# Optimization experiments

Hardware: AMD Instinct MI355X
Metric: run time of the kernel (lower is better)

## Reference

```python
import jax, jax.numpy as jnp
import numpy as np

B, S, H = 8, 32, 2048          # batch, block (query) length, hidden size
NH, NKV, HD = 16, 2, 128       # attention heads, kv heads, head_dim
KV_LEN = 8192                  # block kv-cache length
GROUPS = NH // NKV
SCALE = HD ** -0.5


def rotate_half(x):
    x1, x2 = jnp.split(x, 2, axis=-1)
    return jnp.concatenate((-x2, x1), axis=-1)


def setup_inputs() -> dict:
    key = jax.random.key(0)
    ks = jax.random.split(key, 12)
    inv_freq = 1.0 / (10000.0 ** (jnp.arange(0, HD, 2, dtype=jnp.float32) / HD))
    pos = jnp.arange(S, dtype=jnp.float32)[:, None] * inv_freq[None, :]  # [S, HD/2]
    ang = jnp.concatenate([pos, pos], axis=-1)                           # [S, HD]
    cos = jnp.broadcast_to(jnp.cos(ang)[None], (B, S, HD))
    sin = jnp.broadcast_to(jnp.sin(ang)[None], (B, S, HD))
    s = 0.02
    return {
        'hidden_states': jax.random.normal(ks[0], (B, S, H), jnp.float32),
        'cos': cos,
        'sin': sin,
        'k_cache': jax.random.normal(ks[1], (B, NKV, KV_LEN, HD), jnp.float32),
        'v_cache': jax.random.normal(ks[2], (B, NKV, KV_LEN, HD), jnp.float32),
        'attention_mask': jnp.zeros((B, 1, S, KV_LEN), jnp.float32),
        'replace_position': 4096,
        'q_w': jax.random.normal(ks[3], (H, NH * HD), jnp.float32) * s,
        'q_b': jax.random.normal(ks[4], (NH * HD,), jnp.float32) * s,
        'k_w': jax.random.normal(ks[5], (H, NKV * HD), jnp.float32) * s,
        'k_b': jax.random.normal(ks[6], (NKV * HD,), jnp.float32) * s,
        'v_w': jax.random.normal(ks[7], (H, NKV * HD), jnp.float32) * s,
        'v_b': jax.random.normal(ks[8], (NKV * HD,), jnp.float32) * s,
        'o_w': jax.random.normal(ks[9], (NH * HD, H), jnp.float32) * s,
    }


def reference(hidden_states, cos, sin, k_cache, v_cache, attention_mask,
              replace_position, q_w, q_b, k_w, k_b, v_w, v_b, o_w):
    # fused QKV projections -> [B, heads, S, HD]
    q = (hidden_states @ q_w + q_b).reshape(B, S, NH, HD).transpose(0, 2, 1, 3)
    k = (hidden_states @ k_w + k_b).reshape(B, S, NKV, HD).transpose(0, 2, 1, 3)
    v = (hidden_states @ v_w + v_b).reshape(B, S, NKV, HD).transpose(0, 2, 1, 3)

    # RoPE (cos/sin unsqueezed on the head dim)
    c = cos[:, None]  # [B,1,S,HD]
    s_ = sin[:, None]
    q = q * c + rotate_half(q) * s_
    k = k * c + rotate_half(k) * s_

    # block KV-cache in-place update at replace_position
    k_all = jax.lax.dynamic_update_slice(k_cache, k, (0, 0, replace_position, 0))
    v_all = jax.lax.dynamic_update_slice(v_cache, v, (0, 0, replace_position, 0))

    # GQA: expand kv heads to match attention heads
    k_all = jnp.repeat(k_all, GROUPS, axis=1)  # [B,NH,KV,HD]
    v_all = jnp.repeat(v_all, GROUPS, axis=1)

    # SDPA with additive mask (is_causal=False)
    scores = jnp.einsum('bhqd,bhkd->bhqk', q, k_all) * SCALE + attention_mask
    probs = jax.nn.softmax(scores, axis=-1)
    attn = jnp.einsum('bhqk,bhkd->bhqd', probs, v_all)  # [B,NH,S,HD]

    out = attn.transpose(0, 2, 1, 3).reshape(B, S, NH * HD)
    return out @ o_w
```

## Files before the change

### kernel.cpp

```cpp
#include <hip/hip_runtime.h>
#include <hip/hip_bf16.h>

#define B_    8
#define S_    32
#define H_    2048
#define NH_   16
#define NKV_  2
#define HD_   128
#define KV_   8192
#define G_    8
#define M_    256
#define NQKV  2560
#define NSP   16
#define KT_   64
#define NT_   8
#define SCALE_ 0.08838834764831845f
#define CFIX_  8.0f
#define LOG2E_ 1.4426950408889634f
#define SCALE2_ (SCALE_*LOG2E_)

typedef __bf16 bf16x8 __attribute__((ext_vector_type(8)));
typedef float  f32x4  __attribute__((ext_vector_type(4)));
typedef float  f32x16 __attribute__((ext_vector_type(16)));

__device__ __forceinline__ unsigned short f2b(float f){
  unsigned u = __float_as_uint(f);
  u = u + 0x7FFFu + ((u>>16)&1u);
  return (unsigned short)(u>>16);
}
__device__ __forceinline__ float b2f(unsigned short h){
  return __uint_as_float(((unsigned)h)<<16);
}
__device__ __forceinline__ unsigned cvtpk(float lo, float hi){
  unsigned r;
  asm("v_cvt_pk_bf16_f32 %0, %1, %2" : "=v"(r) : "v"(lo), "v"(hi));
  return r;
}
__device__ __forceinline__ float fexp2(float x){
#if __has_builtin(__builtin_amdgcn_exp2f)
  return __builtin_amdgcn_exp2f(x);
#else
  return __expf(x * 0.6931471805599453f);
#endif
}
__device__ __forceinline__ bf16x8 ld_frag(const unsigned short* p){
  union { uint4 u; bf16x8 b; } cv;
  cv.u = *(const uint4*)p;
  return cv.b;
}
__device__ __forceinline__ f32x4 mf(bf16x8 a, bf16x8 b, f32x4 c){
  return __builtin_amdgcn_mfma_f32_16x16x32_bf16(a, b, c, 0, 0, 0);
}
__device__ __forceinline__ f32x16 mf32(bf16x8 a, bf16x8 b, f32x16 c){
  return __builtin_amdgcn_mfma_f32_32x32x16_bf16(a, b, c, 0, 0, 0);
}
__device__ __forceinline__ int swiK(int row, int col){
  return row*128 + (col ^ ((((row)&15) ^ ((row>>1)&8)) << 3));
}
__device__ __forceinline__ int swiV(int row, int col){
  return row*64 + (col ^ (((row)&7) << 3));
}

__global__ __launch_bounds__(256) void k_gemm_qkv(
    const float* __restrict__ A,
    const float* __restrict__ qw, const float* __restrict__ kw, const float* __restrict__ vw,
    const float* __restrict__ qbv, const float* __restrict__ kbv, const float* __restrict__ vbv,
    float* __restrict__ rawp)
{
  __shared__ unsigned short As[64][56];
  __shared__ unsigned short Bs[64][56];
  const int n0 = blockIdx.x*64, m0 = blockIdx.y*64, kz = blockIdx.z;
  const float* W; const float* bias; int ldw, wc0;
  if(n0 < 2048)      { W=qw; bias=qbv; ldw=2048; wc0=n0; }
  else if(n0 < 2304) { W=kw; bias=kbv; ldw=256;  wc0=n0-2048; }
  else               { W=vw; bias=vbv; ldw=256;  wc0=n0-2304; }
  const int t = threadIdx.x, lane = t&63, wid = t>>6;
  const int wr = wid>>1, wc = wid&1, l15 = lane&15, lq = lane>>4;
  const int ar = t>>2,  ac = (t&3)*8;
  const int bk = t>>5,  bn = (t&31)*2;
  f32x4 acc[2][2] = {};
  for(int k0 = kz*512; k0 < kz*512 + 512; k0 += 32){
    __syncthreads();
    { const float4 a0 = *(const float4*)(A + (m0+ar)*2048 + k0 + ac);
      const float4 a1 = *(const float4*)(A + (m0+ar)*2048 + k0 + ac + 4);
      uint4 w4; w4.x=cvtpk(a0.x,a0.y); w4.y=cvtpk(a0.z,a0.w);
                w4.z=cvtpk(a1.x,a1.y); w4.w=cvtpk(a1.z,a1.w);
      *(uint4*)(&As[ar][ac]) = w4; }
    #pragma unroll
    for(int p=0;p<4;p++){
      const int kk = bk + p*8;
      const float2 wv = *(const float2*)(W + (long)(k0+kk)*ldw + wc0 + bn);
      Bs[bn  ][kk] = f2b(wv.x);
      Bs[bn+1][kk] = f2b(wv.y);
    }
    __syncthreads();
    const bf16x8 a0 = ld_frag(&As[wr*32      + l15][lq*8]);
    const bf16x8 a1 = ld_frag(&As[wr*32 + 16 + l15][lq*8]);
    const bf16x8 b0 = ld_frag(&Bs[wc*32      + l15][lq*8]);
    const bf16x8 b1 = ld_frag(&Bs[wc*32 + 16 + l15][lq*8]);
    acc[0][0] = mf(a0,b0,acc[0][0]);
    acc[0][1] = mf(a0,b1,acc[0][1]);
    acc[1][0] = mf(a1,b0,acc[1][0]);
    acc[1][1] = mf(a1,b1,acc[1][1]);
  }
  float* out = rawp + (long)kz*M_*NQKV;
  #pragma unroll
  for(int mi=0;mi<2;mi++)
    #pragma unroll
    for(int nj=0;nj<2;nj++){
      const int col = n0 + wc*32 + nj*16 + l15;
      const float bv = kz ? 0.f : bias[wc0 + wc*32 + nj*16 + l15];
      #pragma unroll
      for(int rr=0;rr<4;rr++){
        const int row = m0 + wr*32 + mi*16 + lq*4 + rr;
        out[row*NQKV + col] = acc[mi][nj][rr] + bv;
      }
    }
}

__global__ __launch_bounds__(128) void k_rope(
    const float* __restrict__ rawp, const float* __restrict__ cosb, const float* __restrict__ sinb,
    unsigned short* __restrict__ Qb, float* __restrict__ KnF, float* __restrict__ VnF)
{
  const int r = blockIdx.x, hh = blockIdx.y, d = threadIdx.x;
  const int b = r>>5, s = r&31;
  const long MN = (long)M_*NQKV;
  const float cv = cosb[(b*S_+s)*HD_ + d];
  const float sv = sinb[(b*S_+s)*HD_ + d];
  const int dp = (d<64)? d+64 : d-64;
  #define RAW4(c) (rawp[r*NQKV+(c)] + rawp[MN+r*NQKV+(c)] + rawp[2*MN+r*NQKV+(c)] + rawp[3*MN+r*NQKV+(c)])
  if(hh < 16){
    const float x  = RAW4(hh*HD_ + d);
    const float xo = RAW4(hh*HD_ + dp);
    const float y  = x*cv + ((d<64)? -xo : xo)*sv;
    const int kvh = hh>>3, g = hh&7;
    Qb[((long)(b*NKV_+kvh)*M_ + g*S_ + s)*HD_ + d] = f2b(y);
  } else if(hh < 18){
    const int kvh = hh-16;
    const float x  = RAW4(2048 + kvh*HD_ + d);
    const float xo = RAW4(2048 + kvh*HD_ + dp);
    KnF[((long)(b*NKV_+kvh)*S_ + s)*HD_ + d] = x*cv + ((d<64)? -xo : xo)*sv;
  } else {
    const int kvh = hh-18;
    VnF[((long)(b*NKV_+kvh)*S_ + s)*HD_ + d] = RAW4(2304 + kvh*HD_ + d);
  }
  #undef RAW4
}

__global__ __launch_bounds__(256) void k_mswz(const float* __restrict__ mask,
                                              float* __restrict__ msw){
  const int g = blockIdx.x*256 + threadIdx.x;
  const int b = g >> 16, q = (g>>11)&31, c4 = g & 2047;
  const int kv = c4*4;
  const int sp = kv>>9, tt = (kv>>6)&7, kvt = (kv>>5)&1, r4 = (kv>>3)&3, hi = (kv>>2)&1;
  const int lane = q + 32*hi;
  float4 v = *(const float4*)(mask + ((long)b*S_ + q)*KV_ + kv);
  v.x = (v.x - CFIX_)*LOG2E_; v.y = (v.y - CFIX_)*LOG2E_;
  v.z = (v.z - CFIX_)*LOG2E_; v.w = (v.w - CFIX_)*LOG2E_;
  const long dst = ((((long)(b*NSP+sp)*NT_ + tt)*64 + lane)*8 + kvt*4 + r4);
  *(float4*)(msw + dst*4) = v;
}

__global__ __launch_bounds__(512, 2) void k_attn(
    const unsigned short* __restrict__ Qb,
    const float* __restrict__ KnF, const float* __restrict__ VnF,
    const float* __restrict__ kc, const float* __restrict__ vc,
    const float* __restrict__ msw, const int* __restrict__ rpp,
    unsigned short* __restrict__ num, float* __restrict__ lbuf)
{
  __shared__ __align__(16) unsigned short lds[2][2][KT_*128];
  const int sp = blockIdx.x, kvh = blockIdx.y, b = blockIdx.z;
  const int bk = b*NKV_ + kvh;
  const int rp = *rpp;
  const int t = threadIdx.x, lane = t&63, wid = t>>6;
  const int l31 = lane&31, hi = lane>>5;
  const int kvbase = sp*(KV_/NSP);
  const int krow = t>>3, kc0 = (t&7)*16;
  const int vhd  = t&127, vkq = t>>7;
  const int cbsK = (hi*8) ^ ((((l31)&15) ^ ((l31>>1)&8)) << 3);
  const int cbsV = (hi*8) ^ (((l31)&7) << 3);
  const int rowK = l31*128, rowV = l31*64;
  const int wk0 = swiK(krow, kc0), wk1 = swiK(krow, kc0+8);
  const int wv0 = swiV(vhd, vkq*16), wv1 = swiV(vhd, vkq*16+8);

  bf16x8 qf[8];
  { const unsigned short* qp = Qb + ((long)bk*M_ + wid*32 + l31)*HD_;
    #pragma unroll
    for(int ks=0;ks<8;ks++) qf[ks] = ld_frag(qp + ks*16 + hi*8); }

  float4 vK4[4];
  float  vV[16];
  float4 vM[8];
  const float4* mbase = (const float4*)msw + ((long)(b*NSP+sp)*NT_)*64*8 + lane*8;

  auto loadK = [&](int tt){
    const int kvr = kvbase + tt*KT_ + krow;
    const float* kp = (kvr>=rp && kvr<rp+S_)
        ? (KnF + ((long)bk*S_ + (kvr-rp))*HD_ + kc0)
        : (kc  + ((long)bk*KV_ + kvr)*HD_ + kc0);
    #pragma unroll
    for(int i=0;i<4;i++) vK4[i] = *(const float4*)(kp + i*4);
  };
  auto loadV = [&](int tt){
    #pragma unroll
    for(int m=0;m<16;m++){
      const int kvr = kvbase + tt*KT_ + vkq*16 + m;
      const float* vp = (kvr>=rp && kvr<rp+S_)
          ? (VnF + ((long)bk*S_ + (kvr-rp))*HD_)
          : (vc  + ((long)bk*KV_ + kvr)*HD_);
      vV[m] = vp[vhd];
    }
  };
  auto loadM = [&](int tt){
    const float4* mp = mbase + (long)tt*64*8;
    #pragma unroll
    for(int j=0;j<8;j++) vM[j] = mp[j];
  };
  auto writeK = [&](int bb){
    unsigned short* Sb = &lds[bb][0][0];
    uint4 w4;
    w4.x = cvtpk(vK4[0].x, vK4[0].y);  w4.y = cvtpk(vK4[0].z, vK4[0].w);
    w4.z = cvtpk(vK4[1].x, vK4[1].y);  w4.w = cvtpk(vK4[1].z, vK4[1].w);
    *(uint4*)(Sb + wk0) = w4;
    w4.x = cvtpk(vK4[2].x, vK4[2].y);  w4.y = cvtpk(vK4[2].z, vK4[2].w);
    w4.z = cvtpk(vK4[3].x, vK4[3].y);  w4.w = cvtpk(vK4[3].z, vK4[3].w);
    *(uint4*)(Sb + wk1) = w4;
  };
  auto writeV = [&](int bb){
    unsigned short* Sb = &lds[bb][1][0];
    uint4 w4;
    w4.x = cvtpk(vV[0], vV[1]);   w4.y = cvtpk(vV[2], vV[3]);
    w4.z = cvtpk(vV[4], vV[5]);   w4.w = cvtpk(vV[6], vV[7]);
    *(uint4*)(Sb + wv0) = w4;
    w4.x = cvtpk(vV[8], vV[9]);   w4.y = cvtpk(vV[10], vV[11]);
    w4.z = cvtpk(vV[12], vV[13]); w4.w = cvtpk(vV[14], vV[15]);
    *(uint4*)(Sb + wv1) = w4;
  };

  loadK(0); loadV(0);
  writeK(0); writeV(0);
  __syncthreads();

  f32x16 oc[4] = {};
  float l_run = 0.f;

  for(int tt=0; tt<NT_; tt++){
    const int cur = tt&1;
    loadM(tt);
    if(tt<NT_-1){ loadK(tt+1); loadV(tt+1); }
    f32x16 sc[2] = {};
    { const unsigned short* Sk = &lds[cur][0][0];
      __builtin_amdgcn_s_setprio(1);
      #pragma unroll
      for(int ks=0;ks<8;ks++){
        #pragma unroll
        for(int kvt=0;kvt<2;kvt++)
          sc[kvt] = mf32(ld_frag(Sk + rowK + kvt*4096 + (cbsK ^ (ks*16))), qf[ks], sc[kvt]);
      }
      __builtin_amdgcn_s_setprio(0);
    }
    float psum = 0.f;
    #pragma unroll
    for(int kvt=0;kvt<2;kvt++){
      #pragma unroll
      for(int r4=0;r4<4;r4++){
        const float4 mk = vM[kvt*4+r4];
        const float p0 = fexp2(fmaf(sc[kvt][r4*4+0], SCALE2_, mk.x));
        const float p1 = fexp2(fmaf(sc[kvt][r4*4+1], SCALE2_, mk.y));
        const float p2 = fexp2(fmaf(sc[kvt][r4*4+2], SCALE2_, mk.z));
        const float p3 = fexp2(fmaf(sc[kvt][r4*4+3], SCALE2_, mk.w));
        sc[kvt][r4*4+0]=p0; sc[kvt][r4*4+1]=p1;
        sc[kvt][r4*4+2]=p2; sc[kvt][r4*4+3]=p3;
        psum += (p0+p1)+(p2+p3);
      }
    }
    l_run += psum;
    unsigned w_[2][4][2];
    #pragma unroll
    for(int kvt=0;kvt<2;kvt++)
      #pragma unroll
      for(int r4=0;r4<4;r4++){
        w_[kvt][r4][0] = cvtpk(sc[kvt][r4*4+0], sc[kvt][r4*4+1]);
        w_[kvt][r4][1] = cvtpk(sc[kvt][r4*4+2], sc[kvt][r4*4+3]);
      }
    { const unsigned short* Sv = &lds[cur][1][0];
      __builtin_amdgcn_s_setprio(1);
      #pragma unroll
      for(int kvs=0;kvs<4;kvs++){
        const int kvt = kvs>>1, k2 = (kvs&1)*2;
        const unsigned wa0 = w_[kvt][k2  ][0], wa1 = w_[kvt][k2  ][1];
        const unsigned wb0 = w_[kvt][k2+1][0], wb1 = w_[kvt][k2+1][1];
        const unsigned own0 = hi? wb0:wa0, own1 = hi? wb1:wa1;
        const unsigned snd0 = hi? wa0:wb0, snd1 = hi? wa1:wb1;
        const unsigned rcv0 = __shfl_xor(snd0, 32, 64);
        const unsigned rcv1 = __shfl_xor(snd1, 32, 64);
        union{ unsigned u[4]; bf16x8 v; } ap;
        ap.u[0] = hi? rcv0:own0;  ap.u[1] = hi? rcv1:own1;
        ap.u[2] = hi? own0:rcv0;  ap.u[3] = hi? own1:rcv1;
        #pragma unroll
        for(int ht=0;ht<4;ht++)
          oc[ht] = mf32(ap.v, ld_frag(Sv + rowV + ht*2048 + (cbsV ^ (kvs*16))), oc[ht]);
      }
      __builtin_amdgcn_s_setprio(0);
    }
    if(tt<NT_-1){ writeK(cur^1); writeV(cur^1); }
    __syncthreads();
  }

  const float l_tot = l_run + __shfl_xor(l_run, 32, 64);
  if(lane < 32){
    lbuf[((long)bk*NSP + sp)*M_ + wid*32 + lane] = l_tot;
  }
  unsigned short* np_ = num + (((long)bk*NSP + sp)*M_ + wid*32)*HD_;
  #pragma unroll
  for(int ht=0;ht<4;ht++)
    #pragma unroll
    for(int r4=0;r4<4;r4++)
      #pragma unroll
      for(int rr=0;rr<4;rr++){
        const int q = rr + 8*r4 + 4*hi;
        np_[(long)q*HD_ + ht*32 + l31] = f2b(oc[ht][r4*4+rr]);
      }
}

__global__ __launch_bounds__(128) void k_comb(
    const unsigned short* __restrict__ num, const float* __restrict__ lbuf,
    unsigned short* __restrict__ attnb)
{
  const int q = blockIdx.x, kvh = blockIdx.y, b = blockIdx.z, d = threadIdx.x;
  const int bk = b*NKV_ + kvh;
  float den = 0.f, acc = 0.f;
  #pragma unroll
  for(int c=0;c<NSP;c++){
    const long ix = ((long)bk*NSP + c)*M_ + q;
    den += lbuf[ix];
    acc += b2f(num[ix*HD_ + d]);
  }
  const int g = q>>5, s = q&31, h = kvh*G_ + g;
  attnb[((long)(b*S_+s))*2048 + h*HD_ + d] = f2b(acc/den);
}

__global__ __launch_bounds__(256) void k_gemm_o(
    const unsigned short* __restrict__ A,
    const float* __restrict__ W,
    float* __restrict__ owsp)
{
  __shared__ unsigned short As[64][56];
  __shared__ unsigned short Bs[64][56];
  const int n0 = blockIdx.x*64, m0 = blockIdx.y*64, kz = blockIdx.z;
  const int t = threadIdx.x, lane = t&63, wid = t>>6;
  const int wr = wid>>1, wc = wid&1, l15 = lane&15, lq = lane>>4;
  const int ar = t>>2,  ac = (t&3)*8;
  const int bk = t>>5,  bn = (t&31)*2;
  f32x4 acc[2][2] = {};
  for(int k0 = kz*512; k0 < kz*512 + 512; k0 += 32){
    __syncthreads();
    *(uint4*)(&As[ar][ac]) = *(const uint4*)(A + (m0+ar)*2048 + k0 + ac);
    #pragma unroll
    for(int p=0;p<4;p++){
      const int kk = bk + p*8;
      const float2 wv = *(const float2*)(W + (long)(k0+kk)*2048 + n0 + bn);
      Bs[bn  ][kk] = f2b(wv.x);
      Bs[bn+1][kk] = f2b(wv.y);
    }
    __syncthreads();
    const bf16x8 a0 = ld_frag(&As[wr*32      + l15][lq*8]);
    const bf16x8 a1 = ld_frag(&As[wr*32 + 16 + l15][lq*8]);
    const bf16x8 b0 = ld_frag(&Bs[wc*32      + l15][lq*8]);
    const bf16x8 b1 = ld_frag(&Bs[wc*32 + 16 + l15][lq*8]);
    acc[0][0] = mf(a0,b0,acc[0][0]);
    acc[0][1] = mf(a0,b1,acc[0][1]);
    acc[1][0] = mf(a1,b0,acc[1][0]);
    acc[1][1] = mf(a1,b1,acc[1][1]);
  }
  float* out = owsp + (long)kz*M_*2048;
  #pragma unroll
  for(int mi=0;mi<2;mi++)
    #pragma unroll
    for(int nj=0;nj<2;nj++){
      const int col = n0 + wc*32 + nj*16 + l15;
      #pragma unroll
      for(int rr=0;rr<4;rr++){
        const int row = m0 + wr*32 + mi*16 + lq*4 + rr;
        out[row*2048 + col] = acc[mi][nj][rr];
      }
    }
}

__global__ __launch_bounds__(256) void k_ored(const float* __restrict__ a,
                                              float* __restrict__ out){
  const int i = (blockIdx.x*256 + threadIdx.x)*4;
  const long MN = (long)M_*2048;
  const float4 x = *(const float4*)(a + i);
  const float4 y = *(const float4*)(a + MN + i);
  const float4 z = *(const float4*)(a + 2*MN + i);
  const float4 w = *(const float4*)(a + 3*MN + i);
  float4 o; o.x=(x.x+y.x)+(z.x+w.x); o.y=(x.y+y.y)+(z.y+w.y);
            o.z=(x.z+y.z)+(z.z+w.z); o.w=(x.w+y.w)+(z.w+w.w);
  *(float4*)(out + i) = o;
}

extern "C" void kernel_launch(void* const* d_in, const int* in_sizes, int n_in,
                              void* d_out, int out_size, void* d_ws, size_t ws_size,
                              hipStream_t stream){
  (void)in_sizes; (void)n_in; (void)out_size; (void)ws_size;
  const float* hs   = (const float*)d_in[0];
  const float* cosb = (const float*)d_in[1];
  const float* sinb = (const float*)d_in[2];
  const float* kc   = (const float*)d_in[3];
  const float* vc   = (const float*)d_in[4];
  const float* mask = (const float*)d_in[5];
  const int*   rp   = (const int*)  d_in[6];
  const float* qw   = (const float*)d_in[7];
  const float* qb   = (const float*)d_in[8];
  const float* kw   = (const float*)d_in[9];
  const float* kb   = (const float*)d_in[10];
  const float* vw   = (const float*)d_in[11];
  const float* vb   = (const float*)d_in[12];
  const float* ow   = (const float*)d_in[13];
  char* ws = (char*)d_ws;
  float*          rawp  = (float*)         (ws + 0);
  unsigned short* Qb    = (unsigned short*)(ws + 10485760);
  float*          KnF   = (float*)         (ws + 11534336);
  float*          VnF   = (float*)         (ws + 11796480);
  unsigned short* attnb = (unsigned short*)(ws + 12058624);
  float*          lbuf  = (float*)         (ws + 13107200);
  unsigned short* num   = (unsigned short*)(ws + 13369344);
  float*          owsp  = (float*)         (ws + 30146560);
  float*          msw   = (float*)         (ws + 38535168);
  float* outp = (float*)d_out;

  k_gemm_qkv<<<dim3(40,4,4),     dim3(256),  0, stream>>>(hs, qw,kw,vw, qb,kb,vb, rawp);
  k_mswz    <<<dim3(2048),       dim3(256),  0, stream>>>(mask, msw);
  k_rope    <<<dim3(256,20),     dim3(128),  0, stream>>>(rawp, cosb, sinb, Qb, KnF, VnF);
  k_attn    <<<dim3(NSP,2,8),    dim3(512),  0, stream>>>(Qb, KnF, VnF, kc, vc, msw, rp, num, lbuf);
  k_comb    <<<dim3(256,2,8),    dim3(128),  0, stream>>>(num, lbuf, attnb);
  k_gemm_o  <<<dim3(32,4,4),     dim3(256),  0, stream>>>(attnb, ow, owsp);
  k_ored    <<<dim3(512),        dim3(256),  0, stream>>>(owsp, outp);
}
```

Before: 99.21 us.

## Stage weight K-slices in LDS once and sweep all M tiles per block

The QKV and output-projection GEMMs now have each block convert a 256x64 fp32 weight slice to bf16 in shared memory once, then loop over all four 64-row M tiles, rather than re-reading the weight for every M tile. Split-K rises from 4 to 8 so the grid stays reasonably wide, and the rope and output-reduction kernels now sum 8 partial buffers. This aims to cut repeated fp32 weight reads from global memory. In exchange it doubles partial-sum write and read traffic, leaves fewer blocks per launch, and requires a larger workspace.

```diff
diff --git a/kernel.cpp b/kernel.cpp
--- a/kernel.cpp
+++ b/kernel.cpp
@@ -14,6 +14,7 @@
 #define NSP   16
 #define KT_   64
 #define NT_   8
+#define NKZ   8
 #define SCALE_ 0.08838834764831845f
 #define CFIX_  8.0f
 #define LOG2E_ 1.4426950408889634f
@@ -67,9 +68,10 @@
     const float* __restrict__ qbv, const float* __restrict__ kbv, const float* __restrict__ vbv,
     float* __restrict__ rawp)
 {
-  __shared__ unsigned short As[64][56];
-  __shared__ unsigned short Bs[64][56];
-  const int n0 = blockIdx.x*64, m0 = blockIdx.y*64, kz = blockIdx.z;
+  __shared__ unsigned short Bs[64][264];
+  __shared__ unsigned short As[64][40];
+  const int n0 = blockIdx.x*64, kz = blockIdx.y;
+  const int kb = kz*256;
   const float* W; const float* bias; int ldw, wc0;
   if(n0 < 2048)      { W=qw; bias=qbv; ldw=2048; wc0=n0; }
   else if(n0 < 2304) { W=kw; bias=kbv; ldw=256;  wc0=n0-2048; }
@@ -78,44 +80,50 @@
   const int wr = wid>>1, wc = wid&1, l15 = lane&15, lq = lane>>4;
   const int ar = t>>2,  ac = (t&3)*8;
   const int bk = t>>5,  bn = (t&31)*2;
-  f32x4 acc[2][2] = {};
-  for(int k0 = kz*512; k0 < kz*512 + 512; k0 += 32){
-    __syncthreads();
-    { const float4 a0 = *(const float4*)(A + (m0+ar)*2048 + k0 + ac);
-      const float4 a1 = *(const float4*)(A + (m0+ar)*2048 + k0 + ac + 4);
-      uint4 w4; w4.x=cvtpk(a0.x,a0.y); w4.y=cvtpk(a0.z,a0.w);
-                w4.z=cvtpk(a1.x,a1.y); w4.w=cvtpk(a1.z,a1.w);
-      *(uint4*)(&As[ar][ac]) = w4; }
+  #pragma unroll
+  for(int ks8=0; ks8<8; ++ks8){
     #pragma unroll
     for(int p=0;p<4;p++){
-      const int kk = bk + p*8;
-      const float2 wv = *(const float2*)(W + (long)(k0+kk)*ldw + wc0 + bn);
+      const int kk = ks8*32 + bk + p*8;
+      const float2 wv = *(const float2*)(W + (long)(kb+kk)*ldw + wc0 + bn);
       Bs[bn  ][kk] = f2b(wv.x);
       Bs[bn+1][kk] = f2b(wv.y);
     }
-    __syncthreads();
-    const bf16x8 a0 = ld_frag(&As[wr*32      + l15][lq*8]);
-    const bf16x8 a1 = ld_frag(&As[wr*32 + 16 + l15][lq*8]);
-    const bf16x8 b0 = ld_frag(&Bs[wc*32      + l15][lq*8]);
-    const bf16x8 b1 = ld_frag(&Bs[wc*32 + 16 + l15][lq*8]);
-    acc[0][0] = mf(a0,b0,acc[0][0]);
-    acc[0][1] = mf(a0,b1,acc[0][1]);
-    acc[1][0] = mf(a1,b0,acc[1][0]);
-    acc[1][1] = mf(a1,b1,acc[1][1]);
   }
   float* out = rawp + (long)kz*M_*NQKV;
-  #pragma unroll
-  for(int mi=0;mi<2;mi++)
-    #pragma unroll
-    for(int nj=0;nj<2;nj++){
-      const int col = n0 + wc*32 + nj*16 + l15;
-      const float bv = kz ? 0.f : bias[wc0 + wc*32 + nj*16 + l15];
-      #pragma unroll
-      for(int rr=0;rr<4;rr++){
-        const int row = m0 + wr*32 + mi*16 + lq*4 + rr;
-        out[row*NQKV + col] = acc[mi][nj][rr] + bv;
-      }
-    }
+  for(int m0i=0; m0i<4; ++m0i){
+    const int m0 = m0i*64;
+    f32x4 acc[2][2] = {};
+    for(int k0=0; k0<256; k0+=32){
+      __syncthreads();
+      { const float4 a0 = *(const float4*)(A + (m0+ar)*2048 + kb + k0 + ac);
+        const float4 a1 = *(const float4*)(A + (m0+ar)*2048 + kb + k0 + ac + 4);
+        uint4 w4; w4.x=cvtpk(a0.x,a0.y); w4.y=cvtpk(a0.z,a0.w);
+                  w4.z=cvtpk(a1.x,a1.y); w4.w=cvtpk(a1.z,a1.w);
+        *(uint4*)(&As[ar][ac]) = w4; }
+      __syncthreads();
+      const bf16x8 a0 = ld_frag(&As[wr*32      + l15][lq*8]);
+      const bf16x8 a1 = ld_frag(&As[wr*32 + 16 + l15][lq*8]);
+      const bf16x8 b0 = ld_frag(&Bs[wc*32      + l15][k0 + lq*8]);
+      const bf16x8 b1 = ld_frag(&Bs[wc*32 + 16 + l15][k0 + lq*8]);
+      acc[0][0] = mf(a0,b0,acc[0][0]);
+      acc[0][1] = mf(a0,b1,acc[0][1]);
+      acc[1][0] = mf(a1,b0,acc[1][0]);
+      acc[1][1] = mf(a1,b1,acc[1][1]);
+    }
+    #pragma unroll
+    for(int mi=0;mi<2;mi++)
+      #pragma unroll
+      for(int nj=0;nj<2;nj++){
+        const int col = n0 + wc*32 + nj*16 + l15;
+        const float bv = kz ? 0.f : bias[wc0 + wc*32 + nj*16 + l15];
+        #pragma unroll
+        for(int rr=0;rr<4;rr++){
+          const int row = m0 + wr*32 + mi*16 + lq*4 + rr;
+          out[row*NQKV + col] = acc[mi][nj][rr] + bv;
+        }
+      }
+  }
 }
 
 __global__ __launch_bounds__(128) void k_rope(
@@ -128,23 +136,27 @@
   const float cv = cosb[(b*S_+s)*HD_ + d];
   const float sv = sinb[(b*S_+s)*HD_ + d];
   const int dp = (d<64)? d+64 : d-64;
-  #define RAW4(c) (rawp[r*NQKV+(c)] + rawp[MN+r*NQKV+(c)] + rawp[2*MN+r*NQKV+(c)] + rawp[3*MN+r*NQKV+(c)])
+  auto raw8 = [&](int c)->float{
+    float s_ = 0.f;
+    #pragma unroll
+    for(int z=0; z<NKZ; ++z) s_ += rawp[(long)z*MN + r*NQKV + c];
+    return s_;
+  };
   if(hh < 16){
-    const float x  = RAW4(hh*HD_ + d);
-    const float xo = RAW4(hh*HD_ + dp);
+    const float x  = raw8(hh*HD_ + d);
+    const float xo = raw8(hh*HD_ + dp);
     const float y  = x*cv + ((d<64)? -xo : xo)*sv;
     const int kvh = hh>>3, g = hh&7;
     Qb[((long)(b*NKV_+kvh)*M_ + g*S_ + s)*HD_ + d] = f2b(y);
   } else if(hh < 18){
     const int kvh = hh-16;
-    const float x  = RAW4(2048 + kvh*HD_ + d);
-    const float xo = RAW4(2048 + kvh*HD_ + dp);
+    const float x  = raw8(2048 + kvh*HD_ + d);
+    const float xo = raw8(2048 + kvh*HD_ + dp);
     KnF[((long)(b*NKV_+kvh)*S_ + s)*HD_ + d] = x*cv + ((d<64)? -xo : xo)*sv;
   } else {
     const int kvh = hh-18;
-    VnF[((long)(b*NKV_+kvh)*S_ + s)*HD_ + d] = RAW4(2304 + kvh*HD_ + d);
-  }
-  #undef RAW4
+    VnF[((long)(b*NKV_+kvh)*S_ + s)*HD_ + d] = raw8(2304 + kvh*HD_ + d);
+  }
 }
 
 __global__ __launch_bounds__(256) void k_mswz(const float* __restrict__ mask,
@@ -345,58 +357,65 @@
     const float* __restrict__ W,
     float* __restrict__ owsp)
 {
-  __shared__ unsigned short As[64][56];
-  __shared__ unsigned short Bs[64][56];
-  const int n0 = blockIdx.x*64, m0 = blockIdx.y*64, kz = blockIdx.z;
+  __shared__ unsigned short Bs[64][264];
+  __shared__ unsigned short As[64][40];
+  const int n0 = blockIdx.x*64, kz = blockIdx.y;
+  const int kb = kz*256;
   const int t = threadIdx.x, lane = t&63, wid = t>>6;
   const int wr = wid>>1, wc = wid&1, l15 = lane&15, lq = lane>>4;
   const int ar = t>>2,  ac = (t&3)*8;
   const int bk = t>>5,  bn = (t&31)*2;
-  f32x4 acc[2][2] = {};
-  for(int k0 = kz*512; k0 < kz*512 + 512; k0 += 32){
-    __syncthreads();
-    *(uint4*)(&As[ar][ac]) = *(const uint4*)(A + (m0+ar)*2048 + k0 + ac);
+  #pragma unroll
+  for(int ks8=0; ks8<8; ++ks8){
     #pragma unroll
     for(int p=0;p<4;p++){
-      const int kk = bk + p*8;
-      const float2 wv = *(const float2*)(W + (long)(k0+kk)*2048 + n0 + bn);
+      const int kk = ks8*32 + bk + p*8;
+      const float2 wv = *(const float2*)(W + (long)(kb+kk)*2048 + n0 + bn);
       Bs[bn  ][kk] = f2b(wv.x);
       Bs[bn+1][kk] = f2b(wv.y);
     }
-    __syncthreads();
-    const bf16x8 a0 = ld_frag(&As[wr*32      + l15][lq*8]);
-    const bf16x8 a1 = ld_frag(&As[wr*32 + 16 + l15][lq*8]);
-    const bf16x8 b0 = ld_frag(&Bs[wc*32      + l15][lq*8]);
-    const bf16x8 b1 = ld_frag(&Bs[wc*32 + 16 + l15][lq*8]);
-    acc[0][0] = mf(a0,b0,acc[0][0]);
-    acc[0][1] = mf(a0,b1,acc[0][1]);
-    acc[1][0] = mf(a1,b0,acc[1][0]);
-    acc[1][1] = mf(a1,b1,acc[1][1]);
   }
   float* out = owsp + (long)kz*M_*2048;
-  #pragma unroll
-  for(int mi=0;mi<2;mi++)
-    #pragma unroll
-    for(int nj=0;nj<2;nj++){
-      const int col = n0 + wc*32 + nj*16 + l15;
-      #pragma unroll
-      for(int rr=0;rr<4;rr++){
-        const int row = m0 + wr*32 + mi*16 + lq*4 + rr;
-        out[row*2048 + col] = acc[mi][nj][rr];
-      }
-    }
+  for(int m0i=0; m0i<4; ++m0i){
+    const int m0 = m0i*64;
+    f32x4 acc[2][2] = {};
+    for(int k0=0; k0<256; k0+=32){
+      __syncthreads();
+      *(uint4*)(&As[ar][ac]) = *(const uint4*)(A + (m0+ar)*2048 + kb + k0 + ac);
+      __syncthreads();
+      const bf16x8 a0 = ld_frag(&As[wr*32      + l15][lq*8]);
+      const bf16x8 a1 = ld_frag(&As[wr*32 + 16 + l15][lq*8]);
+      const bf16x8 b0 = ld_frag(&Bs[wc*32      + l15][k0 + lq*8]);
+      const bf16x8 b1 = ld_frag(&Bs[wc*32 + 16 + l15][k0 + lq*8]);
+      acc[0][0] = mf(a0,b0,acc[0][0]);
+      acc[0][1] = mf(a0,b1,acc[0][1]);
+      acc[1][0] = mf(a1,b0,acc[1][0]);
+      acc[1][1] = mf(a1,b1,acc[1][1]);
+    }
+    #pragma unroll
+    for(int mi=0;mi<2;mi++)
+      #pragma unroll
+      for(int nj=0;nj<2;nj++){
+        const int col = n0 + wc*32 + nj*16 + l15;
+        #pragma unroll
+        for(int rr=0;rr<4;rr++){
+          const int row = m0 + wr*32 + mi*16 + lq*4 + rr;
+          out[row*2048 + col] = acc[mi][nj][rr];
+        }
+      }
+  }
 }
 
 __global__ __launch_bounds__(256) void k_ored(const float* __restrict__ a,
                                               float* __restrict__ out){
   const int i = (blockIdx.x*256 + threadIdx.x)*4;
   const long MN = (long)M_*2048;
-  const float4 x = *(const float4*)(a + i);
-  const float4 y = *(const float4*)(a + MN + i);
-  const float4 z = *(const float4*)(a + 2*MN + i);
-  const float4 w = *(const float4*)(a + 3*MN + i);
-  float4 o; o.x=(x.x+y.x)+(z.x+w.x); o.y=(x.y+y.y)+(z.y+w.y);
-            o.z=(x.z+y.z)+(z.z+w.z); o.w=(x.w+y.w)+(z.w+w.w);
+  float4 o = *(const float4*)(a + i);
+  #pragma unroll
+  for(int z=1; z<NKZ; ++z){
+    const float4 x = *(const float4*)(a + (long)z*MN + i);
+    o.x += x.x; o.y += x.y; o.z += x.z; o.w += x.w;
+  }
   *(float4*)(out + i) = o;
 }
 
@@ -420,21 +439,21 @@
   const float* ow   = (const float*)d_in[13];
   char* ws = (char*)d_ws;
   float*          rawp  = (float*)         (ws + 0);
-  unsigned short* Qb    = (unsigned short*)(ws + 10485760);
-  float*          KnF   = (float*)         (ws + 11534336);
-  float*          VnF   = (float*)         (ws + 11796480);
-  unsigned short* attnb = (unsigned short*)(ws + 12058624);
-  float*          lbuf  = (float*)         (ws + 13107200);
-  unsigned short* num   = (unsigned short*)(ws + 13369344);
-  float*          owsp  = (float*)         (ws + 30146560);
-  float*          msw   = (float*)         (ws + 38535168);
+  unsigned short* Qb    = (unsigned short*)(ws + 20971520);
+  float*          KnF   = (float*)         (ws + 22020096);
+  float*          VnF   = (float*)         (ws + 22282240);
+  unsigned short* attnb = (unsigned short*)(ws + 22544384);
+  float*          lbuf  = (float*)         (ws + 23592960);
+  unsigned short* num   = (unsigned short*)(ws + 23855104);
+  float*          owsp  = (float*)         (ws + 40632320);
+  float*          msw   = (float*)         (ws + 57409536);
   float* outp = (float*)d_out;
 
-  k_gemm_qkv<<<dim3(40,4,4),     dim3(256),  0, stream>>>(hs, qw,kw,vw, qb,kb,vb, rawp);
+  k_gemm_qkv<<<dim3(40,NKZ),     dim3(256),  0, stream>>>(hs, qw,kw,vw, qb,kb,vb, rawp);
   k_mswz    <<<dim3(2048),       dim3(256),  0, stream>>>(mask, msw);
   k_rope    <<<dim3(256,20),     dim3(128),  0, stream>>>(rawp, cosb, sinb, Qb, KnF, VnF);
   k_attn    <<<dim3(NSP,2,8),    dim3(512),  0, stream>>>(Qb, KnF, VnF, kc, vc, msw, rp, num, lbuf);
   k_comb    <<<dim3(256,2,8),    dim3(128),  0, stream>>>(num, lbuf, attnb);
-  k_gemm_o  <<<dim3(32,4,4),     dim3(256),  0, stream>>>(attnb, ow, owsp);
+  k_gemm_o  <<<dim3(32,NKZ),     dim3(256),  0, stream>>>(attnb, ow, owsp);
   k_ored    <<<dim3(512),        dim3(256),  0, stream>>>(owsp, outp);
 }
```

Result: slower. 105.2 us (+6.1%).
